# Kernel optimization log

Measured on AMD Instinct MI355X. Metric: run time of the kernel, lower is better.

The kernel has to match this reference:

```python
import jax, jax.numpy as jnp
import numpy as np

CMP_STRIDE, CMP_BLOCK = 16, 32
SEL_BLOCK, SEL_COUNT = 64, 16
WINDOW = 512
B, S, HQ, HKV, D = 1, 1536, 16, 2, 128


def setup_inputs() -> dict:
    key = jax.random.key(0)
    ks = jax.random.split(key, 10)
    f = lambda k_, sh, sc=1.0: jax.random.normal(k_, sh, jnp.float32) * sc
    return {
        "q": f(ks[0], (B * S, HQ, D)),
        "k": f(ks[1], (B * S, HKV, D)),
        "v": f(ks[2], (B * S, HKV, D)),
        "Wk": f(ks[3], (CMP_BLOCK * D, D), 0.02),
        "bk": jnp.zeros((D,), jnp.float32),
        "Wv": f(ks[4], (CMP_BLOCK * D, D), 0.02),
        "bv": jnp.zeros((D,), jnp.float32),
        "pek": f(ks[5], (CMP_BLOCK, D), 0.02),
        "pev": f(ks[6], (CMP_BLOCK, D), 0.02),
        "Wg": f(ks[7], (D, 3), 0.02),
        "bg": jnp.zeros((3,), jnp.float32),
        "cu_seqlens": jnp.array([0, S], jnp.int32),
        "max_seqlen": S,
    }


def _compress(x, W, b, pe):
    # x: [B,T,H,D] -> overlapping blocks (stride 16, len 32) -> learned linear per block
    Bb, T, H, Dd = x.shape
    Tc = (T - CMP_BLOCK) // CMP_STRIDE + 1
    idx = jnp.arange(Tc)[:, None] * CMP_STRIDE + jnp.arange(CMP_BLOCK)[None, :]
    blk = x[:, idx] + pe[None, None, :, None, :]          # [B,Tc,L,H,D] + intra-block pos emb
    blk = blk.transpose(0, 1, 3, 2, 4).reshape(Bb, Tc, H, CMP_BLOCK * Dd)
    return blk @ W + b                                    # [B,Tc,H,D]


def _msoftmax(logits, mask):
    # masked softmax; fully-masked rows produce zeros
    logits = jnp.where(mask, logits, jnp.finfo(logits.dtype).min)
    m = jnp.max(logits, -1, keepdims=True)
    e = jnp.exp(logits - m) * mask
    return e / jnp.maximum(e.sum(-1, keepdims=True), 1e-9)


def _forward(q, k, v, Wk, bk, Wv, bv, pek, pev, Wg, bg):
    scale = 1.0 / jnp.sqrt(jnp.float32(D))
    G = HQ // HKV
    qb = q.reshape(B, S, HQ, D)
    kb = k.reshape(B, S, HKV, D)
    vb = v.reshape(B, S, HKV, D)
    pos = jnp.arange(S)[:, None]

    # ---- stage 1: compressed-KV attention ----
    ck = _compress(kb, Wk, bk, pek)                        # [B,Tc,HKV,D]
    cv = _compress(vb, Wv, bv, pev)
    Tc = ck.shape[1]
    ckh = jnp.repeat(ck, G, axis=2)
    cvh = jnp.repeat(cv, G, axis=2)
    cl = jnp.einsum('bshd,bthd->bhst', qb, ckh) * scale    # [B,HQ,S,Tc]
    cmask = (jnp.arange(Tc)[None, :] * CMP_STRIDE + CMP_BLOCK - 1) <= pos  # block fully visible
    cp = _msoftmax(cl, cmask[None, None])
    cmp_o = jnp.einsum('bhst,bthd->bshd', cp, cvh)

    # ---- stage 2: pooled-score top-k block selection ----
    score = cp.reshape(B, HKV, G, S, Tc).sum(2)            # sum over GQA group -> [B,HKV,S,Tc]
    Kp = SEL_BLOCK // CMP_STRIDE + 1                       # AvgPool1d kernel = 5
    St = SEL_BLOCK // CMP_STRIDE                           # stride = 4
    P = CMP_BLOCK // CMP_STRIDE - 2                        # padding = 0
    n_out = -(-(Tc + 2 * P - Kp) // St) + 1                # ceil_mode=True
    widx = jnp.arange(n_out)[:, None] * St - P + jnp.arange(Kp)[None, :]
    inb = (widx >= 0) & (widx < Tc)
    cnt = ((widx >= -P) & (widx < Tc + P)).sum(-1)         # count_include_pad divisor
    gathered = jnp.where(inb[None, None, None], score[..., jnp.clip(widx, 0, Tc - 1)], 0.0)
    pooled = gathered.sum(-1) / cnt                        # [B,HKV,S,n_out]
    _, top_idx = jax.lax.top_k(pooled, SEL_COUNT)          # [B,HKV,S,SEL_COUNT]

    # ---- stage 3: block-sparse selected attention + sliding window ----
    n_kblk = S // SEL_BLOCK
    blk_sel = (top_idx[..., None] == jnp.arange(n_kblk)).any(-2)   # [B,HKV,S,n_kblk]
    key_blk = jnp.arange(S) // SEL_BLOCK
    causal = jnp.arange(S)[None, :] <= pos                 # [S,S]
    sel_mask = jnp.take(blk_sel, key_blk, axis=-1) & causal[None, None]
    sel_mask = jnp.repeat(sel_mask, G, axis=1)             # [B,HQ,S,S]
    win_mask = causal & (jnp.arange(S)[None, :] > pos - WINDOW)

    kh = jnp.repeat(kb, G, axis=2)
    vh = jnp.repeat(vb, G, axis=2)
    logits = jnp.einsum('bshd,buhd->bhsu', qb, kh) * scale # [B,HQ,S,S]
    sel_o = jnp.einsum('bhsu,buhd->bshd', _msoftmax(logits, sel_mask), vh)
    win_o = jnp.einsum('bhsu,buhd->bshd', _msoftmax(logits, win_mask[None, None]), vh)

    # ---- gated combine of three branches ----
    gate = jax.nn.sigmoid(jnp.einsum('bshd,de->bshe', qb, Wg) + bg)  # [B,S,HQ,3]
    o = gate[..., 0:1] * sel_o + gate[..., 1:2] * win_o + gate[..., 2:3] * cmp_o
    return o.reshape(-1, HQ, D)


def reference(q, k, v, Wk, bk, Wv, bv, pek, pev, Wg, bg, cu_seqlens, max_seqlen):
    return _forward(q, k, v, Wk, bk, Wv, bv, pek, pev, Wg, bg)
```

## Files before the change

### kernel.cpp

```cpp
#include <hip/hip_runtime.h>


#define S_LEN 1536
#define HQ    16
#define HKV   2
#define DH    128
#define TC    95
#define WIN   512
#define TQ    16
#define SCALE 0.08838834764831845f
#define M_INIT 4.0f
#define THR    8.0f

typedef _Float16 f16;
typedef f16   f16x4 __attribute__((ext_vector_type(4)));
typedef f16   f16x8 __attribute__((ext_vector_type(8)));
typedef float f32x4 __attribute__((ext_vector_type(4)));

__device__ inline f16x8 cvt8(float4 A, float4 B) {
    f16x8 h;
    h[0]=(f16)A.x; h[1]=(f16)A.y; h[2]=(f16)A.z; h[3]=(f16)A.w;
    h[4]=(f16)B.x; h[5]=(f16)B.y; h[6]=(f16)B.z; h[7]=(f16)B.w;
    return h;
}
__device__ inline f16x8 cvt8s(float4 A, float4 B, float s) {
    f16x8 h;
    h[0]=(f16)(A.x*s); h[1]=(f16)(A.y*s); h[2]=(f16)(A.z*s); h[3]=(f16)(A.w*s);
    h[4]=(f16)(B.x*s); h[5]=(f16)(B.y*s); h[6]=(f16)(B.z*s); h[7]=(f16)(B.w*s);
    return h;
}

__global__ __launch_bounds__(256) void compress_init_kernel(
    const float* __restrict__ bk, const float* __restrict__ bv,
    float* __restrict__ ck, float* __restrict__ cv)
{
    int i = blockIdx.x * 256 + threadIdx.x;
    int which = i >= TC*HKV*DH;
    int j = i - which*(TC*HKV*DH);
    int d = j & 127;
    (which ? cv : ck)[j] = (which ? bv : bk)[d];
}

__global__ __launch_bounds__(256) void compress_partial_kernel(
    const float* __restrict__ kin, const float* __restrict__ vin,
    const float* __restrict__ Wk,  const float* __restrict__ Wv,
    const float* __restrict__ pek, const float* __restrict__ pev,
    float* __restrict__ ck, float* __restrict__ cv)
{
    const int t0    = blockIdx.x * 5;
    const int kv    = blockIdx.y >> 1;
    const int which = blockIdx.y & 1;
    const int kc    = blockIdx.z;
    const float* __restrict__ x  = which ? vin : kin;
    const float* __restrict__ W  = which ? Wv  : Wk;
    const float* __restrict__ pe = which ? pev : pek;
    float* __restrict__ outp     = which ? cv  : ck;
    const int tid = threadIdx.x;
    const int hh  = tid >> 7;
    const int d   = tid & 127;

    __shared__ float xs[2][5][128];
    __shared__ float racc[5][128];
    float acc[5] = {0.f, 0.f, 0.f, 0.f, 0.f};

    #pragma unroll
    for (int il = 0; il < 2; ++il) {
        const int l = kc*4 + hh*2 + il;
        float p = pe[l*DH + d];
        #pragma unroll
        for (int tt = 0; tt < 5; ++tt) {
            int row = (t0 + tt)*16 + l;
            xs[hh][tt][d] = x[(row*HKV + kv)*DH + d] + p;
        }
        __syncthreads();
        const float* wcol = W + l*DH*DH + d;
        #pragma unroll 8
        for (int dd = 0; dd < 128; ++dd) {
            float wv = wcol[dd*DH];
            #pragma unroll
            for (int tt = 0; tt < 5; ++tt) acc[tt] += xs[hh][tt][dd] * wv;
        }
        __syncthreads();
    }
    if (hh == 1) {
        #pragma unroll
        for (int tt = 0; tt < 5; ++tt) racc[tt][d] = acc[tt];
    }
    __syncthreads();
    if (hh == 0) {
        #pragma unroll
        for (int tt = 0; tt < 5; ++tt)
            atomicAdd(&outp[((t0 + tt)*HKV + kv)*DH + d], acc[tt] + racc[tt][d]);
    }
}

__global__ __launch_bounds__(256) void cmp_attn_mfma(
    const float* __restrict__ q, const float* __restrict__ ck,
    const float* __restrict__ cv, float* __restrict__ cmp_o,
    unsigned int* __restrict__ blk_mask)
{
    const int s0   = blockIdx.x * 8;
    const int kv   = blockIdx.y;
    const int tid  = threadIdx.x;
    const int w    = tid >> 6;
    const int lane = tid & 63;
    const int quad = lane >> 4;
    const int l4   = lane & 15;

    __shared__ __align__(16) char BUF[52736];
    f16* __restrict__ CKH = (f16*)BUF;
    f16* __restrict__ CKL = (f16*)(BUF + 26112);
    f16* __restrict__ CVR = (f16*)BUF;
    f16* __restrict__ CVT = (f16*)(BUF + 26112);
    f16*   __restrict__ Pw = (f16*)BUF + w*1664;
    float* __restrict__ SC = (float*)(BUF + 13312);
    float* __restrict__ PO = (float*)(BUF + 16384);

    #pragma unroll
    for (int i = 0; i < 6; ++i) {
        int idx = i*256 + tid;
        int row = idx >> 4, cg = idx & 15;
        float4 A = make_float4(0.f,0.f,0.f,0.f), B = A;
        if (row < TC) {
            const float* src = ck + ((size_t)(row*HKV + kv))*DH + cg*8;
            A = *(const float4*)src; B = *(const float4*)(src + 4);
        }
        f16x8 h = cvt8(A, B);
        f16x8 l;
        l[0]=(f16)(A.x-(float)h[0]); l[1]=(f16)(A.y-(float)h[1]);
        l[2]=(f16)(A.z-(float)h[2]); l[3]=(f16)(A.w-(float)h[3]);
        l[4]=(f16)(B.x-(float)h[4]); l[5]=(f16)(B.y-(float)h[5]);
        l[6]=(f16)(B.z-(float)h[6]); l[7]=(f16)(B.w-(float)h[7]);
        *(f16x8*)&CKH[row*136 + cg*8] = h;
        *(f16x8*)&CKL[row*136 + cg*8] = l;
    }

    const int qrow_local = w*16 + l4;
    const int sA = s0 + (qrow_local >> 3);
    const int hA = qrow_local & 7;
    f16x8 aqh[4], aql[4];
    {
        const float* qrow = q + ((size_t)(sA*HQ + kv*8 + hA))*DH;
        #pragma unroll
        for (int ks = 0; ks < 4; ++ks) {
            float4 A = *(const float4*)(qrow + ks*32 + quad*8);
            float4 B = *(const float4*)(qrow + ks*32 + quad*8 + 4);
            A.x*=SCALE; A.y*=SCALE; A.z*=SCALE; A.w*=SCALE;
            B.x*=SCALE; B.y*=SCALE; B.z*=SCALE; B.w*=SCALE;
            f16x8 h = cvt8(A, B);
            f16x8 l;
            l[0]=(f16)(A.x-(float)h[0]); l[1]=(f16)(A.y-(float)h[1]);
            l[2]=(f16)(A.z-(float)h[2]); l[3]=(f16)(A.w-(float)h[3]);
            l[4]=(f16)(B.x-(float)h[4]); l[5]=(f16)(B.y-(float)h[5]);
            l[6]=(f16)(B.z-(float)h[6]); l[7]=(f16)(B.w-(float)h[7]);
            aqh[ks] = h; aql[ks] = l;
        }
    }
    __syncthreads();

    f32x4 sc[6];
    #pragma unroll
    for (int nt = 0; nt < 6; ++nt) {
        sc[nt] = (f32x4){0.f,0.f,0.f,0.f};
        #pragma unroll
        for (int ks = 0; ks < 4; ++ks) {
            f16x8 bh = *(const f16x8*)&CKH[(nt*16 + l4)*136 + ks*32 + quad*8];
            f16x8 bl = *(const f16x8*)&CKL[(nt*16 + l4)*136 + ks*32 + quad*8];
            sc[nt] = __builtin_amdgcn_mfma_f32_16x16x32_f16(aqh[ks], bh, sc[nt], 0, 0, 0);
            sc[nt] = __builtin_amdgcn_mfma_f32_16x16x32_f16(aql[ks], bh, sc[nt], 0, 0, 0);
            sc[nt] = __builtin_amdgcn_mfma_f32_16x16x32_f16(aqh[ks], bl, sc[nt], 0, 0, 0);
        }
    }
    __syncthreads();

    #pragma unroll
    for (int i = 0; i < 6; ++i) {
        int idx = i*256 + tid;
        int row = idx >> 4, cg = idx & 15;
        float4 A = make_float4(0.f,0.f,0.f,0.f), B = A;
        if (row < TC) {
            const float* src = cv + ((size_t)(row*HKV + kv))*DH + cg*8;
            A = *(const float4*)src; B = *(const float4*)(src + 4);
        }
        *(f16x8*)&CVR[row*136 + cg*8] = cvt8(A, B);
    }
    __syncthreads();
    #pragma unroll
    for (int i = 0; i < 6; ++i) {
        int idx = i*256 + tid;
        int d = idx & 127, tc = idx >> 7;
        f16x8 h;
        #pragma unroll
        for (int j = 0; j < 8; ++j) h[j] = CVR[(tc*8 + j)*136 + d];
        *(f16x8*)&CVT[d*104 + tc*8] = h;
    }
    __syncthreads();

    const int s_q = s0 + 2*w + (quad >> 1);
    const int nv  = (s_q >= 31) ? (((s_q - 31) >> 4) + 1) : 0;
    bool valid[6];
    #pragma unroll
    for (int nt = 0; nt < 6; ++nt) valid[nt] = (nt*16 + l4) < nv;

    float pn[6][4];
    float lsum[4];
    #pragma unroll
    for (int r = 0; r < 4; ++r) {
        float m = -3.4e38f;
        #pragma unroll
        for (int nt = 0; nt < 6; ++nt) m = fmaxf(m, valid[nt] ? sc[nt][r] : -3.4e38f);
        #pragma unroll
        for (int off = 1; off < 16; off <<= 1) m = fmaxf(m, __shfl_xor(m, off));
        float s = 0.f;
        #pragma unroll
        for (int nt = 0; nt < 6; ++nt) {
            float e = valid[nt] ? __expf(sc[nt][r] - m) : 0.f;
            pn[nt][r] = e;
            s += e;
        }
        #pragma unroll
        for (int off = 1; off < 16; off <<= 1) s += __shfl_xor(s, off);
        const float inv = 1.f / fmaxf(s, 1e-9f);
        #pragma unroll
        for (int nt = 0; nt < 6; ++nt) pn[nt][r] *= inv;
        lsum[r] = s;
    }
    (void)lsum;

    #pragma unroll
    for (int nt = 0; nt < 6; ++nt) {
        #pragma unroll
        for (int r = 0; r < 4; ++r)
            Pw[(quad*4 + r)*104 + nt*16 + l4] = (f16)pn[nt][r];
        float scq = pn[nt][0] + pn[nt][1] + pn[nt][2] + pn[nt][3];
        scq += __shfl_xor(scq, 16);
        if ((quad & 1) == 0)
            SC[(w*2 + (quad >> 1))*96 + nt*16 + l4] = scq;
    }

    {
        int qi = lane >> 5;
        int o  = lane & 31;
        bool sel = false;
        if (o < 24) {
            float acc = 0.f, cnt = 0.f;
            #pragma unroll
            for (int j = 0; j < 5; ++j) {
                int wd = o*4 + j;
                if (wd < TC) { acc += SC[(w*2 + qi)*96 + wd]; cnt += 1.f; }
            }
            PO[(w*2 + qi)*24 + o] = acc / cnt;
        }
        if (o < 24) {
            float pvv = PO[(w*2 + qi)*24 + o];
            int rank = 0;
            #pragma unroll
            for (int j = 0; j < 24; ++j) {
                float pj = PO[(w*2 + qi)*24 + j];
                rank += ((pj > pvv) || (pj == pvv && j < o)) ? 1 : 0;
            }
            sel = rank < 16;
        }
        unsigned long long b = __ballot(sel);
        if (lane == 0) {
            blk_mask[kv*S_LEN + s0 + 2*w]     = (unsigned int)(b & 0xFFFFFFull);
            blk_mask[kv*S_LEN + s0 + 2*w + 1] = (unsigned int)((b >> 32) & 0xFFFFFFull);
        }
    }

    f32x4 O[8];
    #pragma unroll
    for (int nf = 0; nf < 8; ++nf) O[nf] = (f32x4){0.f,0.f,0.f,0.f};
    #pragma unroll
    for (int ks2 = 0; ks2 < 3; ++ks2) {
        f16x8 ap = *(const f16x8*)&Pw[l4*104 + ks2*32 + quad*8];
        #pragma unroll
        for (int nf = 0; nf < 8; ++nf) {
            f16x8 bv = *(const f16x8*)&CVT[(nf*16 + l4)*104 + ks2*32 + quad*8];
            O[nf] = __builtin_amdgcn_mfma_f32_16x16x32_f16(ap, bv, O[nf], 0, 0, 0);
        }
    }
    #pragma unroll
    for (int r = 0; r < 4; ++r) {
        const int h_r = (quad & 1)*4 + r;
        const size_t base = ((size_t)(s_q*HQ + kv*8 + h_r))*DH;
        #pragma unroll
        for (int nf = 0; nf < 8; ++nf)
            cmp_o[base + nf*16 + l4] = O[nf][r];
    }
}

__global__ __launch_bounds__(512, 2) void main_attn_split(
    const float* __restrict__ q, const float* __restrict__ kg,
    const float* __restrict__ vg,
    const unsigned int* __restrict__ blk_mask,
    float* __restrict__ po, float* __restrict__ ml,
    int nsplit)
{
    const int t0    = (S_LEN/TQ - 1 - blockIdx.x) * TQ;
    const int kv    = blockIdx.y;
    const int split = blockIdx.z;
    const int tid   = threadIdx.x;
    const int w     = tid >> 6;
    const int lane  = tid & 63;
    const int quad  = lane >> 4;
    const int l4    = lane & 15;
    const int head  = w;

    __shared__ __align__(16) f16 Klds[64*136];
    __shared__ __align__(16) f16 Vt[128*72];
    __shared__ __align__(16) f16 PldsS[8][16*72];
    __shared__ __align__(16) f16 PldsW[8][16*72];
    f16* __restrict__ PwS = PldsS[w];
    f16* __restrict__ PwW = PldsW[w];

    int srow[4]; unsigned selm[4];
    #pragma unroll
    for (int r = 0; r < 4; ++r) {
        srow[r] = t0 + quad*4 + r;
        selm[r] = blk_mask[kv*S_LEN + srow[r]];
    }
    unsigned um = 0;
    for (int i = 0; i < TQ; ++i) um |= blk_mask[kv*S_LEN + t0 + i];

    const int nkb = ((t0 + TQ - 1) >> 6) + 1;
    const int wlo_tile = t0 - WIN + 1;

    unsigned act_all = 0;
    for (int kb2 = 0; kb2 < nkb; ++kb2) {
        bool a = ((um >> kb2) & 1u) || ((kb2*64 + 63) >= wlo_tile);
        if (a) act_all |= (1u << kb2);
    }
    unsigned act = 0;
    {
        int ii = 0;
        for (unsigned t = act_all; t; t &= t - 1, ++ii)
            if (ii % nsplit == split) act |= (t & -t);
    }
    if (act == 0) {
        #pragma unroll
        for (int r = 0; r < 4; ++r) {
            const size_t rh = (size_t)srow[r]*HQ + kv*8 + head;
            const size_t bs = ((size_t)(split*2+0)*S_LEN*HQ + rh)*DH;
            const size_t bw = ((size_t)(split*2+1)*S_LEN*HQ + rh)*DH;
            #pragma unroll
            for (int nf = 0; nf < 8; ++nf) {
                po[bs + nf*16 + l4] = 0.f;
                po[bw + nf*16 + l4] = 0.f;
            }
            if (l4 == 0) {
                const size_t ms = ((size_t)(split*2+0)*S_LEN*HQ + rh)*2;
                const size_t mw = ((size_t)(split*2+1)*S_LEN*HQ + rh)*2;
                ml[ms+0] = -1e30f; ml[ms+1] = 0.f;
                ml[mw+0] = -1e30f; ml[mw+1] = 0.f;
            }
        }
        return;
    }

    f16x8 aq[4];
    {
        const float* qrow = q + ((size_t)(t0 + l4)*HQ + kv*8 + head)*DH;
        #pragma unroll
        for (int ks = 0; ks < 4; ++ks) {
            float4 A = *(const float4*)(qrow + ks*32 + quad*8);
            float4 B = *(const float4*)(qrow + ks*32 + quad*8 + 4);
            aq[ks] = cvt8s(A, B, SCALE);
        }
    }

    f32x4 o_s[8], o_w[8];
    #pragma unroll
    for (int nf = 0; nf < 8; ++nf) {
        o_s[nf] = (f32x4){0.f,0.f,0.f,0.f};
        o_w[nf] = (f32x4){0.f,0.f,0.f,0.f};
    }
    float m_s[4], l_s[4], m_w[4], l_w[4];
    #pragma unroll
    for (int r = 0; r < 4; ++r) { m_s[r]=M_INIT; l_s[r]=0.f; m_w[r]=M_INIT; l_w[r]=0.f; }

    int key_[2], cg_[2], vd_[2], vk_[2];
    #pragma unroll
    for (int i = 0; i < 2; ++i) {
        int idx = i*512 + tid;
        key_[i] = idx >> 4;  cg_[i] = idx & 15;
        vd_[i]  = idx & 127; vk_[i] = idx >> 7;
    }

    float4 pkA[2], pkB[2];
    float  pv[2][8];
    int kb = __builtin_ctz(act); act &= act - 1;
    #pragma unroll
    for (int i = 0; i < 2; ++i) {
        const float* sK = kg + ((size_t)(kb*64 + key_[i])*HKV + kv)*DH + cg_[i]*8;
        pkA[i] = *(const float4*)sK; pkB[i] = *(const float4*)(sK + 4);
        #pragma unroll
        for (int j = 0; j < 8; ++j)
            pv[i][j] = vg[((size_t)(kb*64 + vk_[i]*8 + j)*HKV + kv)*DH + vd_[i]];
    }

    while (true) {
        __syncthreads();
        #pragma unroll
        for (int i = 0; i < 2; ++i)
            *(f16x8*)&Klds[key_[i]*136 + cg_[i]*8] = cvt8(pkA[i], pkB[i]);
        #pragma unroll
        for (int i = 0; i < 2; ++i) {
            f16x8 h;
            #pragma unroll
            for (int j = 0; j < 8; ++j) h[j] = (f16)pv[i][j];
            *(f16x8*)&Vt[vd_[i]*72 + vk_[i]*8] = h;
        }
        __syncthreads();

        const int cur = kb;
        const bool more = (act != 0);
        if (more) {
            kb = __builtin_ctz(act); act &= act - 1;
            #pragma unroll
            for (int i = 0; i < 2; ++i) {
                const float* sK = kg + ((size_t)(kb*64 + key_[i])*HKV + kv)*DH + cg_[i]*8;
                pkA[i] = *(const float4*)sK; pkB[i] = *(const float4*)(sK + 4);
                #pragma unroll
                for (int j = 0; j < 8; ++j)
                    pv[i][j] = vg[((size_t)(kb*64 + vk_[i]*8 + j)*HKV + kv)*DH + vd_[i]];
            }
        }

        f32x4 sc[4];
        #pragma unroll
        for (int nt = 0; nt < 4; ++nt) {
            sc[nt] = (f32x4){0.f,0.f,0.f,0.f};
            #pragma unroll
            for (int ks = 0; ks < 4; ++ks) {
                f16x8 bk = *(const f16x8*)&Klds[(nt*16 + l4)*136 + ks*32 + quad*8];
                sc[nt] = __builtin_amdgcn_mfma_f32_16x16x32_f16(aq[ks], bk, sc[nt], 0, 0, 0);
            }
        }

        const int keyb = cur*64;
        const bool any_sel = (um >> cur) & 1u;
        const bool any_win = (keyb + 63) >= wlo_tile;
        unsigned selb[4];
        #pragma unroll
        for (int r = 0; r < 4; ++r) selb[r] = (selm[r] >> cur) & 1u;

        float lmx_s[4] = {-1e30f,-1e30f,-1e30f,-1e30f};
        float lmx_w[4] = {-1e30f,-1e30f,-1e30f,-1e30f};
        #pragma unroll
        for (int nt = 0; nt < 4; ++nt) {
            int key = keyb + nt*16 + l4;
            #pragma unroll
            for (int r = 0; r < 4; ++r) {
                bool okc = key <= srow[r];
                bool okS = okc && selb[r];
                bool okW = okc && (key > srow[r] - WIN);
                lmx_s[r] = fmaxf(lmx_s[r], okS ? sc[nt][r] : -1e30f);
                lmx_w[r] = fmaxf(lmx_w[r], okW ? sc[nt][r] : -1e30f);
            }
        }

        bool cond = true;
        if (any_sel) {
            #pragma unroll
            for (int r = 0; r < 4; ++r) cond = cond && (lmx_s[r] <= m_s[r] + THR);
        }
        if (any_win) {
            #pragma unroll
            for (int r = 0; r < 4; ++r) cond = cond && (lmx_w[r] <= m_w[r] + THR);
        }
        if (!__all(cond)) {
            if (any_sel) {
                #pragma unroll
                for (int r = 0; r < 4; ++r) {
                    float rm = lmx_s[r];
                    #pragma unroll
                    for (int off = 1; off < 16; off <<= 1)
                        rm = fmaxf(rm, __shfl_xor(rm, off));
                    float nm = fmaxf(m_s[r], rm);
                    float alpha = __expf(m_s[r] - nm);
                    m_s[r] = nm;
                    l_s[r] *= alpha;
                    #pragma unroll
                    for (int nf = 0; nf < 8; ++nf) o_s[nf][r] *= alpha;
                }
            }
            if (any_win) {
                #pragma unroll
                for (int r = 0; r < 4; ++r) {
                    float rm = lmx_w[r];
                    #pragma unroll
                    for (int off = 1; off < 16; off <<= 1)
                        rm = fmaxf(rm, __shfl_xor(rm, off));
                    float nm = fmaxf(m_w[r], rm);
                    float alpha = __expf(m_w[r] - nm);
                    m_w[r] = nm;
                    l_w[r] *= alpha;
                    #pragma unroll
                    for (int nf = 0; nf < 8; ++nf) o_w[nf][r] *= alpha;
                }
            }
        }

        if (any_sel) {
            #pragma unroll
            for (int nt = 0; nt < 4; ++nt) {
                int key = keyb + nt*16 + l4;
                #pragma unroll
                for (int r = 0; r < 4; ++r) {
                    bool ok = (key <= srow[r]) && selb[r];
                    float p = ok ? __expf(sc[nt][r] - m_s[r]) : 0.f;
                    l_s[r] += p;
                    PwS[(quad*4 + r)*72 + nt*16 + l4] = (f16)p;
                }
            }
        }
        if (any_win) {
            #pragma unroll
            for (int nt = 0; nt < 4; ++nt) {
                int key = keyb + nt*16 + l4;
                #pragma unroll
                for (int r = 0; r < 4; ++r) {
                    bool ok = (key <= srow[r]) && (key > srow[r] - WIN);
                    float p = ok ? __expf(sc[nt][r] - m_w[r]) : 0.f;
                    l_w[r] += p;
                    PwW[(quad*4 + r)*72 + nt*16 + l4] = (f16)p;
                }
            }
        }

        if (any_sel) {
            #pragma unroll
            for (int ks2 = 0; ks2 < 2; ++ks2) {
                f16x8 ap = *(const f16x8*)&PwS[l4*72 + ks2*32 + quad*8];
                #pragma unroll
                for (int nf = 0; nf < 8; ++nf) {
                    f16x8 bv = *(const f16x8*)&Vt[(nf*16 + l4)*72 + ks2*32 + quad*8];
                    o_s[nf] = __builtin_amdgcn_mfma_f32_16x16x32_f16(ap, bv, o_s[nf], 0, 0, 0);
                }
            }
        }
        if (any_win) {
            #pragma unroll
            for (int ks2 = 0; ks2 < 2; ++ks2) {
                f16x8 ap = *(const f16x8*)&PwW[l4*72 + ks2*32 + quad*8];
                #pragma unroll
                for (int nf = 0; nf < 8; ++nf) {
                    f16x8 bv = *(const f16x8*)&Vt[(nf*16 + l4)*72 + ks2*32 + quad*8];
                    o_w[nf] = __builtin_amdgcn_mfma_f32_16x16x32_f16(ap, bv, o_w[nf], 0, 0, 0);
                }
            }
        }

        if (!more) break;
    }

    #pragma unroll
    for (int r = 0; r < 4; ++r) {
        #pragma unroll
        for (int off = 1; off < 16; off <<= 1) {
            l_s[r] += __shfl_xor(l_s[r], off);
            l_w[r] += __shfl_xor(l_w[r], off);
        }
    }

    #pragma unroll
    for (int r = 0; r < 4; ++r) {
        const size_t rh = (size_t)srow[r]*HQ + kv*8 + head;
        const size_t bs = ((size_t)(split*2+0)*S_LEN*HQ + rh)*DH;
        const size_t bw = ((size_t)(split*2+1)*S_LEN*HQ + rh)*DH;
        #pragma unroll
        for (int nf = 0; nf < 8; ++nf) {
            po[bs + nf*16 + l4] = o_s[nf][r];
            po[bw + nf*16 + l4] = o_w[nf][r];
        }
        if (l4 == 0) {
            const size_t ms = ((size_t)(split*2+0)*S_LEN*HQ + rh)*2;
            const size_t mw = ((size_t)(split*2+1)*S_LEN*HQ + rh)*2;
            ml[ms+0] = m_s[r]; ml[ms+1] = l_s[r];
            ml[mw+0] = m_w[r]; ml[mw+1] = l_w[r];
        }
    }
}

__global__ __launch_bounds__(256) void combine_kernel(
    const float* __restrict__ q, const float* __restrict__ po,
    const float* __restrict__ ml, const float* __restrict__ Wg,
    const float* __restrict__ bg, float* __restrict__ out, int nsplit)
{
    const int unit = blockIdx.x * 4 + (threadIdx.x >> 6);
    const int lane = threadIdx.x & 63;
    const int row  = unit >> 4;
    const int h    = unit & 15;
    const size_t rh = (size_t)row*HQ + h;

    float p0 = 0.f, p1 = 0.f, p2 = 0.f;
    const float* qrow = q + rh*DH;
    #pragma unroll
    for (int t = 0; t < 2; ++t) {
        int d = t*64 + lane;
        float qv = qrow[d];
        p0 += qv*Wg[d*3+0]; p1 += qv*Wg[d*3+1]; p2 += qv*Wg[d*3+2];
    }
    #pragma unroll
    for (int off = 1; off < 64; off <<= 1) {
        p0 += __shfl_xor(p0, off);
        p1 += __shfl_xor(p1, off);
        p2 += __shfl_xor(p2, off);
    }
    const float g0 = 1.f/(1.f + __expf(-(p0 + bg[0])));
    const float g1 = 1.f/(1.f + __expf(-(p1 + bg[1])));
    const float g2 = 1.f/(1.f + __expf(-(p2 + bg[2])));

    float res0 = 0.f, res1 = 0.f;
    #pragma unroll
    for (int b = 0; b < 2; ++b) {
        float M = -1e30f;
        for (int s = 0; s < nsplit; ++s)
            M = fmaxf(M, ml[((size_t)(s*2+b)*S_LEN*HQ + rh)*2 + 0]);
        float L = 0.f, osum0 = 0.f, osum1 = 0.f;
        for (int s = 0; s < nsplit; ++s) {
            const size_t mlb = ((size_t)(s*2+b)*S_LEN*HQ + rh)*2;
            const float wgt = __expf(ml[mlb+0] - M);
            L += ml[mlb+1] * wgt;
            const size_t ob = ((size_t)(s*2+b)*S_LEN*HQ + rh)*DH;
            osum0 += po[ob + lane]      * wgt;
            osum1 += po[ob + 64 + lane] * wgt;
        }
        const float inv = 1.f / fmaxf(L, 1e-9f);
        const float g = b ? g1 : g0;
        res0 += g * osum0 * inv;
        res1 += g * osum1 * inv;
    }
    const size_t ob = rh*DH;
    out[ob + lane]      = res0 + g2*out[ob + lane];
    out[ob + 64 + lane] = res1 + g2*out[ob + 64 + lane];
}

__global__ __launch_bounds__(256, 2) void main_attn_mfma(
    const float* __restrict__ q, const float* __restrict__ kg,
    const float* __restrict__ vg, const float* cmp_o,
    const unsigned int* __restrict__ blk_mask,
    const float* __restrict__ Wg, const float* __restrict__ bg,
    float* out)
{
    const int t0   = (S_LEN/TQ - 1 - blockIdx.x) * TQ;
    const int kv   = blockIdx.y;
    const int z    = blockIdx.z;
    const int tid  = threadIdx.x;
    const int w    = tid >> 6;
    const int lane = tid & 63;
    const int quad = lane >> 4;
    const int l4   = lane & 15;
    const int head = z*4 + w;

    __shared__ __align__(16) f16 Klds[64*136];
    __shared__ __align__(16) f16 Vrow[64*136];
    __shared__ __align__(16) f16 Vt[128*72];
    __shared__ __align__(16) f16 Plds[4][16*72];
    f16* __restrict__ Pw = Plds[w];

    f16x8 aq[4];
    {
        const float* qrow = q + ((size_t)(t0 + l4)*HQ + kv*8 + head)*DH;
        #pragma unroll
        for (int ks = 0; ks < 4; ++ks) {
            float4 A = *(const float4*)(qrow + ks*32 + quad*8);
            float4 B = *(const float4*)(qrow + ks*32 + quad*8 + 4);
            aq[ks] = cvt8s(A, B, SCALE);
        }
    }

    int srow[4]; unsigned selm[4];
    #pragma unroll
    for (int r = 0; r < 4; ++r) {
        srow[r] = t0 + quad*4 + r;
        selm[r] = blk_mask[kv*S_LEN + srow[r]];
    }
    unsigned um = 0;
    for (int i = 0; i < TQ; ++i) um |= blk_mask[kv*S_LEN + t0 + i];

    f32x4 o_s[8], o_w[8];
    #pragma unroll
    for (int nf = 0; nf < 8; ++nf) {
        o_s[nf] = (f32x4){0.f,0.f,0.f,0.f};
        o_w[nf] = (f32x4){0.f,0.f,0.f,0.f};
    }
    float m_s[4], l_s[4], m_w[4], l_w[4];
    #pragma unroll
    for (int r = 0; r < 4; ++r) { m_s[r]=-1e30f; l_s[r]=0.f; m_w[r]=-1e30f; l_w[r]=0.f; }

    const int nkb = ((t0 + TQ - 1) >> 6) + 1;
    const int wlo_tile = t0 - WIN + 1;

    unsigned act = 0;
    for (int kb2 = 0; kb2 < nkb; ++kb2) {
        bool a = ((um >> kb2) & 1u) || ((kb2*64 + 63) >= wlo_tile);
        if (a) act |= (1u << kb2);
    }

    int key_[4], cg_[4];
    #pragma unroll
    for (int i = 0; i < 4; ++i) { int idx = i*256 + tid; key_[i] = idx >> 4; cg_[i] = idx & 15; }

    float4 pkA[4], pkB[4], pvA[4], pvB[4];
    int kb = __builtin_ctz(act); act &= act - 1;
    #pragma unroll
    for (int i = 0; i < 4; ++i) {
        const float* sK = kg + ((size_t)(kb*64 + key_[i])*HKV + kv)*DH + cg_[i]*8;
        const float* sV = vg + ((size_t)(kb*64 + key_[i])*HKV + kv)*DH + cg_[i]*8;
        pkA[i] = *(const float4*)sK; pkB[i] = *(const float4*)(sK + 4);
        pvA[i] = *(const float4*)sV; pvB[i] = *(const float4*)(sV + 4);
    }

    while (true) {
        __syncthreads();
        #pragma unroll
        for (int i = 0; i < 4; ++i) {
            *(f16x8*)&Klds[key_[i]*136 + cg_[i]*8] = cvt8(pkA[i], pkB[i]);
            *(f16x8*)&Vrow[key_[i]*136 + cg_[i]*8] = cvt8(pvA[i], pvB[i]);
        }
        __syncthreads();

        const int cur = kb;
        const bool more = (act != 0);
        if (more) {
            kb = __builtin_ctz(act); act &= act - 1;
            #pragma unroll
            for (int i = 0; i < 4; ++i) {
                const float* sK = kg + ((size_t)(kb*64 + key_[i])*HKV + kv)*DH + cg_[i]*8;
                const float* sV = vg + ((size_t)(kb*64 + key_[i])*HKV + kv)*DH + cg_[i]*8;
                pkA[i] = *(const float4*)sK; pkB[i] = *(const float4*)(sK + 4);
                pvA[i] = *(const float4*)sV; pvB[i] = *(const float4*)(sV + 4);
            }
        }

        #pragma unroll
        for (int i = 0; i < 4; ++i) {
            int idx = i*256 + tid;
            int d = idx & 127, kg8 = idx >> 7;
            f16x8 h;
            #pragma unroll
            for (int j = 0; j < 8; ++j) h[j] = Vrow[(kg8*8 + j)*136 + d];
            *(f16x8*)&Vt[d*72 + kg8*8] = h;
        }
        __syncthreads();

        f32x4 sc[4];
        #pragma unroll
        for (int nt = 0; nt < 4; ++nt) {
            sc[nt] = (f32x4){0.f,0.f,0.f,0.f};
            #pragma unroll
            for (int ks = 0; ks < 4; ++ks) {
                f16x8 bk = *(const f16x8*)&Klds[(nt*16 + l4)*136 + ks*32 + quad*8];
                sc[nt] = __builtin_amdgcn_mfma_f32_16x16x32_f16(aq[ks], bk, sc[nt], 0, 0, 0);
            }
        }

        const int keyb = cur*64;
        const bool any_sel = (um >> cur) & 1u;
        const bool any_win = (keyb + 63) >= wlo_tile;
        if (any_sel) {
            float rmax[4] = {-1e30f,-1e30f,-1e30f,-1e30f};
            #pragma unroll
            for (int nt = 0; nt < 4; ++nt) {
                int key = keyb + nt*16 + l4;
                #pragma unroll
                for (int r = 0; r < 4; ++r) {
                    bool ok = (key <= srow[r]) && ((selm[r] >> cur) & 1u);
                    rmax[r] = fmaxf(rmax[r], ok ? sc[nt][r] : -1e30f);
                }
            }
            float alpha[4];
            #pragma unroll
            for (int r = 0; r < 4; ++r) {
                #pragma unroll
                for (int off = 1; off < 16; off <<= 1)
                    rmax[r] = fmaxf(rmax[r], __shfl_xor(rmax[r], off));
                float nm = fmaxf(m_s[r], rmax[r]);
                alpha[r] = __expf(m_s[r] - nm);
                m_s[r] = nm;
            }
            float rs[4] = {0.f,0.f,0.f,0.f};
            #pragma unroll
            for (int nt = 0; nt < 4; ++nt) {
                int key = keyb + nt*16 + l4;
                #pragma unroll
                for (int r = 0; r < 4; ++r) {
                    bool ok = (key <= srow[r]) && ((selm[r] >> cur) & 1u);
                    float p = ok ? __expf(sc[nt][r] - m_s[r]) : 0.f;
                    rs[r] += p;
                    Pw[(quad*4 + r)*72 + nt*16 + l4] = (f16)p;
                }
            }
            #pragma unroll
            for (int r = 0; r < 4; ++r) {
                #pragma unroll
                for (int off = 1; off < 16; off <<= 1) rs[r] += __shfl_xor(rs[r], off);
                l_s[r] = l_s[r]*alpha[r] + rs[r];
            }
            #pragma unroll
            for (int nf = 0; nf < 8; ++nf) {
                #pragma unroll
                for (int r = 0; r < 4; ++r) o_s[nf][r] *= alpha[r];
            }
            #pragma unroll
            for (int ks2 = 0; ks2 < 2; ++ks2) {
                f16x8 ap = *(const f16x8*)&Pw[l4*72 + ks2*32 + quad*8];
                #pragma unroll
                for (int nf = 0; nf < 8; ++nf) {
                    f16x8 bv = *(const f16x8*)&Vt[(nf*16 + l4)*72 + ks2*32 + quad*8];
                    o_s[nf] = __builtin_amdgcn_mfma_f32_16x16x32_f16(ap, bv, o_s[nf], 0, 0, 0);
                }
            }
        }
        if (any_win) {
            float rmax[4] = {-1e30f,-1e30f,-1e30f,-1e30f};
            #pragma unroll
            for (int nt = 0; nt < 4; ++nt) {
                int key = keyb + nt*16 + l4;
                #pragma unroll
                for (int r = 0; r < 4; ++r) {
                    bool ok = (key <= srow[r]) && (key > srow[r] - WIN);
                    rmax[r] = fmaxf(rmax[r], ok ? sc[nt][r] : -1e30f);
                }
            }
            float alpha[4];
            #pragma unroll
            for (int r = 0; r < 4; ++r) {
                #pragma unroll
                for (int off = 1; off < 16; off <<= 1)
                    rmax[r] = fmaxf(rmax[r], __shfl_xor(rmax[r], off));
                float nm = fmaxf(m_w[r], rmax[r]);
                alpha[r] = __expf(m_w[r] - nm);
                m_w[r] = nm;
            }
            float rs[4] = {0.f,0.f,0.f,0.f};
            #pragma unroll
            for (int nt = 0; nt < 4; ++nt) {
                int key = keyb + nt*16 + l4;
                #pragma unroll
                for (int r = 0; r < 4; ++r) {
                    bool ok = (key <= srow[r]) && (key > srow[r] - WIN);
                    float p = ok ? __expf(sc[nt][r] - m_w[r]) : 0.f;
                    rs[r] += p;
                    Pw[(quad*4 + r)*72 + nt*16 + l4] = (f16)p;
                }
            }
            #pragma unroll
            for (int r = 0; r < 4; ++r) {
                #pragma unroll
                for (int off = 1; off < 16; off <<= 1) rs[r] += __shfl_xor(rs[r], off);
                l_w[r] = l_w[r]*alpha[r] + rs[r];
            }
            #pragma unroll
            for (int nf = 0; nf < 8; ++nf) {
                #pragma unroll
                for (int r = 0; r < 4; ++r) o_w[nf][r] *= alpha[r];
            }
            #pragma unroll
            for (int ks2 = 0; ks2 < 2; ++ks2) {
                f16x8 ap = *(const f16x8*)&Pw[l4*72 + ks2*32 + quad*8];
                #pragma unroll
                for (int nf = 0; nf < 8; ++nf) {
                    f16x8 bv = *(const f16x8*)&Vt[(nf*16 + l4)*72 + ks2*32 + quad*8];
                    o_w[nf] = __builtin_amdgcn_mfma_f32_16x16x32_f16(ap, bv, o_w[nf], 0, 0, 0);
                }
            }
        }

        if (!more) break;
    }

    float inv_s[4], inv_w[4];
    #pragma unroll
    for (int r = 0; r < 4; ++r) {
        inv_s[r] = 1.f / fmaxf(l_s[r], 1e-9f);
        inv_w[r] = 1.f / fmaxf(l_w[r], 1e-9f);
    }
    float gt[4][3];
    #pragma unroll
    for (int r = 0; r < 4; ++r) {
        float p0 = 0.f, p1 = 0.f, p2 = 0.f;
        const float* qrow = q + ((size_t)srow[r]*HQ + kv*8 + head)*DH + l4*8;
        #pragma unroll
        for (int j = 0; j < 8; ++j) {
            float qv = qrow[j];
            int d = l4*8 + j;
            p0 += qv * Wg[d*3 + 0];
            p1 += qv * Wg[d*3 + 1];
            p2 += qv * Wg[d*3 + 2];
        }
        #pragma unroll
        for (int off = 1; off < 16; off <<= 1) {
            p0 += __shfl_xor(p0, off);
            p1 += __shfl_xor(p1, off);
            p2 += __shfl_xor(p2, off);
        }
        gt[r][0] = 1.f/(1.f + __expf(-(p0 + bg[0])));
        gt[r][1] = 1.f/(1.f + __expf(-(p1 + bg[1])));
        gt[r][2] = 1.f/(1.f + __expf(-(p2 + bg[2])));
    }
    #pragma unroll
    for (int nf = 0; nf < 8; ++nf) {
        int d = nf*16 + l4;
        #pragma unroll
        for (int r = 0; r < 4; ++r) {
            size_t oi = ((size_t)srow[r]*HQ + kv*8 + head)*DH + d;
            float cm = cmp_o[oi];
            out[oi] = gt[r][0]*o_s[nf][r]*inv_s[r]
                    + gt[r][1]*o_w[nf][r]*inv_w[r]
                    + gt[r][2]*cm;
        }
    }
}

extern "C" void kernel_launch(void* const* d_in, const int* in_sizes, int n_in,
                              void* d_out, int out_size, void* d_ws, size_t ws_size,
                              hipStream_t stream) {
    const float* q   = (const float*)d_in[0];
    const float* k   = (const float*)d_in[1];
    const float* v   = (const float*)d_in[2];
    const float* Wk  = (const float*)d_in[3];
    const float* bk  = (const float*)d_in[4];
    const float* Wv  = (const float*)d_in[5];
    const float* bv  = (const float*)d_in[6];
    const float* pek = (const float*)d_in[7];
    const float* pev = (const float*)d_in[8];
    const float* Wg  = (const float*)d_in[9];
    const float* bg  = (const float*)d_in[10];
    float* out = (float*)d_out;

    char* ws = (char*)d_ws;
    float* ck = (float*)ws;
    float* cv = (float*)(ws + 98304);
    unsigned int* blk_mask = (unsigned int*)(ws + 196608);
    float* cmp_o = out;

    compress_init_kernel<<<dim3(190), 256, 0, stream>>>(bk, bv, ck, cv);
    compress_partial_kernel<<<dim3(19, 4, 8), 256, 0, stream>>>(
        k, v, Wk, Wv, pek, pev, ck, cv);
    cmp_attn_mfma<<<dim3(S_LEN/8, HKV), 256, 0, stream>>>(
        q, ck, cv, cmp_o, blk_mask);

    const size_t base      = 208896;
    const size_t o_per_sp  = (size_t)2 * S_LEN * HQ * DH * 4;
    const size_t ml_per_sp = (size_t)2 * S_LEN * HQ * 2 * 4;
    const size_t per_split = o_per_sp + ml_per_sp;

    int nsplit = 0;
    if (ws_size >= base + 3*per_split)      nsplit = 3;
    else if (ws_size >= base + 2*per_split) nsplit = 2;

    if (nsplit >= 2) {
        float* po  = (float*)(ws + base);
        float* mlb = (float*)(ws + base + (size_t)nsplit * o_per_sp);
        main_attn_split<<<dim3(S_LEN/TQ, HKV, nsplit), 512, 0, stream>>>(
            q, k, v, blk_mask, po, mlb, nsplit);
        combine_kernel<<<dim3(S_LEN*HQ/4), 256, 0, stream>>>(
            q, po, mlb, Wg, bg, out, nsplit);
    } else {
        main_attn_mfma<<<dim3(S_LEN/TQ, HKV, 2), 256, 0, stream>>>(
            q, k, v, cmp_o, blk_mask, Wg, bg, out);
    }
}
```

Before: 197.7 us.

## Store split partial outputs in fp16, fuse dual softmax exp, transpose CV directly

Partial attention outputs passed from the split kernel to the combine kernel are now stored as fp16 instead of fp32, halving that round-trip traffic through global memory. The selected and window softmax branches now share one exponential per score, rescaled by exp(m_s - m_w) for the window branch, and both are always computed instead of being gated on any_sel/any_win. The compressed-V transpose now reads global memory directly rather than staging through shared memory with an extra barrier. Risks are reduced precision in the partial sums, possible overflow when m_s is much smaller than m_w, and strided uncoalesced global reads in the CV load.

```diff
diff --git a/kernel.cpp b/kernel.cpp
--- a/kernel.cpp
+++ b/kernel.cpp
@@ -110,7 +110,6 @@
     __shared__ __align__(16) char BUF[52736];
     f16* __restrict__ CKH = (f16*)BUF;
     f16* __restrict__ CKL = (f16*)(BUF + 26112);
-    f16* __restrict__ CVR = (f16*)BUF;
     f16* __restrict__ CVT = (f16*)(BUF + 26112);
     f16*   __restrict__ Pw = (f16*)BUF + w*1664;
     float* __restrict__ SC = (float*)(BUF + 13312);
@@ -176,23 +175,15 @@
     #pragma unroll
     for (int i = 0; i < 6; ++i) {
         int idx = i*256 + tid;
-        int row = idx >> 4, cg = idx & 15;
-        float4 A = make_float4(0.f,0.f,0.f,0.f), B = A;
-        if (row < TC) {
-            const float* src = cv + ((size_t)(row*HKV + kv))*DH + cg*8;
-            A = *(const float4*)src; B = *(const float4*)(src + 4);
-        }
-        *(f16x8*)&CVR[row*136 + cg*8] = cvt8(A, B);
-    }
-    __syncthreads();
-    #pragma unroll
-    for (int i = 0; i < 6; ++i) {
-        int idx = i*256 + tid;
-        int d = idx & 127, tc = idx >> 7;
+        int d = idx & 127, tc8 = idx >> 7;
         f16x8 h;
         #pragma unroll
-        for (int j = 0; j < 8; ++j) h[j] = CVR[(tc*8 + j)*136 + d];
-        *(f16x8*)&CVT[d*104 + tc*8] = h;
+        for (int j = 0; j < 8; ++j) {
+            int row = tc8*8 + j;
+            float v = (row < TC) ? cv[((size_t)(row*HKV + kv))*DH + d] : 0.f;
+            h[j] = (f16)v;
+        }
+        *(f16x8*)&CVT[d*104 + tc8*8] = h;
     }
     __syncthreads();
 
@@ -203,7 +194,6 @@
     for (int nt = 0; nt < 6; ++nt) valid[nt] = (nt*16 + l4) < nv;
 
     float pn[6][4];
-    float lsum[4];
     #pragma unroll
     for (int r = 0; r < 4; ++r) {
         float m = -3.4e38f;
@@ -223,9 +213,7 @@
         const float inv = 1.f / fmaxf(s, 1e-9f);
         #pragma unroll
         for (int nt = 0; nt < 6; ++nt) pn[nt][r] *= inv;
-        lsum[r] = s;
-    }
-    (void)lsum;
+    }
 
     #pragma unroll
     for (int nt = 0; nt < 6; ++nt) {
@@ -294,7 +282,7 @@
     const float* __restrict__ q, const float* __restrict__ kg,
     const float* __restrict__ vg,
     const unsigned int* __restrict__ blk_mask,
-    float* __restrict__ po, float* __restrict__ ml,
+    f16* __restrict__ po, float* __restrict__ ml,
     int nsplit)
 {
     const int t0    = (S_LEN/TQ - 1 - blockIdx.x) * TQ;
@@ -345,8 +333,8 @@
             const size_t bw = ((size_t)(split*2+1)*S_LEN*HQ + rh)*DH;
             #pragma unroll
             for (int nf = 0; nf < 8; ++nf) {
-                po[bs + nf*16 + l4] = 0.f;
-                po[bw + nf*16 + l4] = 0.f;
+                po[bs + nf*16 + l4] = (f16)0.f;
+                po[bw + nf*16 + l4] = (f16)0.f;
             }
             if (l4 == 0) {
                 const size_t ms = ((size_t)(split*2+0)*S_LEN*HQ + rh)*2;
@@ -502,29 +490,25 @@
             }
         }
 
-        if (any_sel) {
+        {
+            float fw[4];
+            #pragma unroll
+            for (int r = 0; r < 4; ++r) fw[r] = __expf(m_s[r] - m_w[r]);
             #pragma unroll
             for (int nt = 0; nt < 4; ++nt) {
                 int key = keyb + nt*16 + l4;
                 #pragma unroll
                 for (int r = 0; r < 4; ++r) {
-                    bool ok = (key <= srow[r]) && selb[r];
-                    float p = ok ? __expf(sc[nt][r] - m_s[r]) : 0.f;
-                    l_s[r] += p;
-                    PwS[(quad*4 + r)*72 + nt*16 + l4] = (f16)p;
-                }
-            }
-        }
-        if (any_win) {
-            #pragma unroll
-            for (int nt = 0; nt < 4; ++nt) {
-                int key = keyb + nt*16 + l4;
-                #pragma unroll
-                for (int r = 0; r < 4; ++r) {
-                    bool ok = (key <= srow[r]) && (key > srow[r] - WIN);
-                    float p = ok ? __expf(sc[nt][r] - m_w[r]) : 0.f;
-                    l_w[r] += p;
-                    PwW[(quad*4 + r)*72 + nt*16 + l4] = (f16)p;
+                    bool okc = key <= srow[r];
+                    bool okS = okc && selb[r];
+                    bool okW = okc && (key > srow[r] - WIN);
+                    float e  = __expf(sc[nt][r] - m_s[r]);
+                    float ps = okS ? e : 0.f;
+                    float pw = okW ? e * fw[r] : 0.f;
+                    l_s[r] += ps;
+                    l_w[r] += pw;
+                    PwS[(quad*4 + r)*72 + nt*16 + l4] = (f16)ps;
+                    PwW[(quad*4 + r)*72 + nt*16 + l4] = (f16)pw;
                 }
             }
         }
@@ -571,8 +555,8 @@
         const size_t bw = ((size_t)(split*2+1)*S_LEN*HQ + rh)*DH;
         #pragma unroll
         for (int nf = 0; nf < 8; ++nf) {
-            po[bs + nf*16 + l4] = o_s[nf][r];
-            po[bw + nf*16 + l4] = o_w[nf][r];
+            po[bs + nf*16 + l4] = (f16)o_s[nf][r];
+            po[bw + nf*16 + l4] = (f16)o_w[nf][r];
         }
         if (l4 == 0) {
             const size_t ms = ((size_t)(split*2+0)*S_LEN*HQ + rh)*2;
@@ -584,7 +568,7 @@
 }
 
 __global__ __launch_bounds__(256) void combine_kernel(
-    const float* __restrict__ q, const float* __restrict__ po,
+    const float* __restrict__ q, const f16* __restrict__ po,
     const float* __restrict__ ml, const float* __restrict__ Wg,
     const float* __restrict__ bg, float* __restrict__ out, int nsplit)
 {
@@ -624,8 +608,8 @@
             const float wgt = __expf(ml[mlb+0] - M);
             L += ml[mlb+1] * wgt;
             const size_t ob = ((size_t)(s*2+b)*S_LEN*HQ + rh)*DH;
-            osum0 += po[ob + lane]      * wgt;
-            osum1 += po[ob + 64 + lane] * wgt;
+            osum0 += (float)po[ob + lane]      * wgt;
+            osum1 += (float)po[ob + 64 + lane] * wgt;
         }
         const float inv = 1.f / fmaxf(L, 1e-9f);
         const float g = b ? g1 : g0;
@@ -944,7 +928,7 @@
         q, ck, cv, cmp_o, blk_mask);
 
     const size_t base      = 208896;
-    const size_t o_per_sp  = (size_t)2 * S_LEN * HQ * DH * 4;
+    const size_t o_per_sp  = (size_t)2 * S_LEN * HQ * DH * 2;
     const size_t ml_per_sp = (size_t)2 * S_LEN * HQ * 2 * 4;
     const size_t per_split = o_per_sp + ml_per_sp;
 
@@ -953,7 +937,7 @@
     else if (ws_size >= base + 2*per_split) nsplit = 2;
 
     if (nsplit >= 2) {
-        float* po  = (float*)(ws + base);
+        f16*   po  = (f16*)(ws + base);
         float* mlb = (float*)(ws + base + (size_t)nsplit * o_per_sp);
         main_attn_split<<<dim3(S_LEN/TQ, HKV, nsplit), 512, 0, stream>>>(
             q, k, v, blk_mask, po, mlb, nsplit);
```

Result: no change. 200.1 us (+1.2%).
